# Kernel tuning notes

Measured on AMD Instinct MI355X. Metric: run time of the kernel, lower is better.

Reference implementation:

```python
import jax, jax.numpy as jnp
import numpy as np

BUCKETS = 16


def conv2d(x, w, b):
    # x: [N, Cin, H, W], w: [Cout, Cin, kh, kw], stride 1, padding 1
    y = jax.lax.conv_general_dilated(
        x, w, window_strides=(1, 1), padding=((1, 1), (1, 1)),
        dimension_numbers=("NCHW", "OIHW", "NCHW"))
    return y + b[None, :, None, None]


def setup_inputs() -> dict:
    key = jax.random.key(0)
    k1, k2, k3, k4, k5 = jax.random.split(key, 5)
    x = jax.random.normal(k1, (32, 64, 112, 112), dtype=jnp.float32)
    W = jax.random.normal(k2, (128, 64, 3, 3), dtype=jnp.float32) * 0.05
    b = jax.random.normal(k3, (128,), dtype=jnp.float32) * 0.05
    b2 = jax.random.normal(k4, (128,), dtype=jnp.float32) * 0.05  # hashed_conv's own bias
    hashed_weights = jax.random.normal(k5, (BUCKETS,), dtype=jnp.float32)
    return {"x": x, "W": W, "b": b, "b2": b2, "hashed_weights": hashed_weights}


def reference(x, W, b, b2, hashed_weights):
    out = conv2d(x, W, b)
    # thresholds derived from min/max of the ORIGINAL weights
    wmax = jnp.max(W)
    wmin = jnp.min(W)
    step = (wmax - wmin) / BUCKETS
    # sequential per-bucket replacement (faithful to in-place loop semantics:
    # values replaced at bucket i are re-compared against later thresholds)
    hw = W
    for i in range(BUCKETS):
        thr = (i + 1) * step + wmin
        hw = jnp.where(hw > thr, hashed_weights[i], hw)
    hashed_out = conv2d(x, hw, b2)
    return (out, hashed_out)
```

## Files before the change

### kernel.cpp

```cpp
#include <hip/hip_runtime.h>
#include <stdint.h>

#define CIN 64
#define HHW 112
#define NPIX 12544
#define COUT 128
#define KTOT 576
#define NBUCKETS 16

typedef __attribute__((ext_vector_type(8))) short s8v;
typedef __attribute__((ext_vector_type(4))) float f4v;
typedef __attribute__((ext_vector_type(8))) unsigned short u8v;

__device__ __forceinline__ unsigned short f2bf(float f) {
  unsigned int u = __float_as_uint(f);
  unsigned int r = (u + 0x7fffu + ((u >> 16) & 1u)) >> 16;
  return (unsigned short)r;
}

__device__ __forceinline__ void gload_lds16(const void* g, void* l) {
  __builtin_amdgcn_global_load_lds(
      (const __attribute__((address_space(1))) unsigned int*)g,
      (__attribute__((address_space(3))) unsigned int*)l, 16, 0, 0);
}

__global__ __launch_bounds__(1024) void hashedconv_prep_kernel(
    const float* __restrict__ W, const float* __restrict__ hashed_w,
    unsigned short* __restrict__ W2, unsigned short* __restrict__ zp) {
  const int NW = COUT * CIN * 9;
  int tid = threadIdx.x;
  if (zp && tid < 128) zp[tid] = 0;
  float vmin = 1e30f, vmax = -1e30f;
  for (int i = tid; i < NW; i += 1024) {
    float v = W[i];
    vmin = fminf(vmin, v);
    vmax = fmaxf(vmax, v);
  }
  #pragma unroll
  for (int off = 32; off > 0; off >>= 1) {
    vmin = fminf(vmin, __shfl_down(vmin, off, 64));
    vmax = fmaxf(vmax, __shfl_down(vmax, off, 64));
  }
  __shared__ float smin[16], smax[16];
  __shared__ float s_wmin, s_step;
  __shared__ float hv[NBUCKETS];
  int wave = tid >> 6, lane = tid & 63;
  if (lane == 0) { smin[wave] = vmin; smax[wave] = vmax; }
  if (tid < NBUCKETS) hv[tid] = hashed_w[tid];
  __syncthreads();
  if (tid == 0) {
    float m = smin[0], M = smax[0];
    #pragma unroll
    for (int i = 1; i < 16; ++i) { m = fminf(m, smin[i]); M = fmaxf(M, smax[i]); }
    s_wmin = m;
    s_step = (M - m) / (float)NBUCKETS;
  }
  __syncthreads();
  float wmin = s_wmin, step = s_step;
  for (int i = tid; i < NW; i += 1024) {
    float v = W[i];
    int co  = i / 576;
    int rem = i - co * 576;
    int cin = rem / 9;
    int off = rem - cin * 9;
    float h = v;
    #pragma unroll
    for (int b = 0; b < NBUCKETS; ++b) {
      float thr = (float)(b + 1) * step + wmin;
      if (h > thr) h = hv[b];
    }
    int oidx = co * KTOT + off * 64 + cin;
    W2[oidx]               = f2bf(v);
    W2[COUT * KTOT + oidx] = f2bf(h);
  }
}

__global__ __launch_bounds__(256) void xpose_kernel(
    const float* __restrict__ x, unsigned short* __restrict__ xb) {
  __shared__ unsigned short t[64][264];
  const int n = blockIdx.y, p0 = blockIdx.x * 256, tid = threadIdx.x;
  const float* xp = x + (size_t)n * CIN * NPIX + p0;
  #pragma unroll
  for (int c = 0; c < 64; ++c)
    t[c][tid] = f2bf(xp[(size_t)c * NPIX + tid]);
  __syncthreads();
  unsigned short* ob = xb + ((size_t)n * NPIX + p0) * 64;
  #pragma unroll
  for (int it = 0; it < 8; ++it) {
    int u = it * 256 + tid;
    int px = u >> 3, slot = u & 7;
    u8v v;
    #pragma unroll
    for (int k = 0; k < 8; ++k) v[k] = t[slot * 8 + k][px];
    *(u8v*)(ob + (size_t)u * 8) = v;
  }
}

#define XS_PIXPAD 352
#define XS_SHORTS (XS_PIXPAD * 64)
#define HALF_SHORTS (128 * 32)

__global__ __launch_bounds__(256, 2) void hashedconv_mfma_kernel(
    const unsigned short* __restrict__ xb, const unsigned short* __restrict__ W2,
    const float* __restrict__ b, const float* __restrict__ b2,
    const unsigned short* __restrict__ zp, float* __restrict__ out,
    size_t out_half) {
  __shared__ __attribute__((aligned(16))) short lds[XS_SHORTS + 4 * HALF_SHORTS];
  short* xs = lds;
  short* ring = lds + XS_SHORTS;

  const int tid = threadIdx.x;
  const int bx = blockIdx.x;
  const int n  = blockIdx.y;
  const int hf = blockIdx.z;
  const int ty = bx / 7, tx = bx - ty * 7;
  const int h0 = ty * 16, w0 = tx * 16;
  const int lane = tid & 63, wv = tid >> 6;
  const int wr = wv >> 1;
  const int wcn = wv & 1;
  const int lrow = lane & 15, g = lane >> 4;

  const unsigned short* Wh = W2 + (size_t)hf * COUT * KTOT;

  #pragma unroll
  for (int it = 0; it < 11; ++it) {
    int u = it * 256 + tid;
    int pix = u >> 3, slot = u & 7;
    int py = pix / 18, px = pix - py * 18;
    int gh = h0 - 1 + py, gw = w0 - 1 + px;
    bool inb = (pix < 324) & (gh >= 0) & (gh < HHW) & (gw >= 0) & (gw < HHW);
    int srcslot = slot ^ (pix & 7);
    const unsigned short* gsrc = inb
        ? xb + (((size_t)n * NPIX + gh * HHW + gw) * 64 + srcslot * 8)
        : zp + srcslot * 8;
    gload_lds16(gsrc, xs + (size_t)(it * 256 + wv * 64) * 8);
  }

  auto stage_half = [&](int h) {
    short* buf = ring + (size_t)(h & 3) * HALF_SHORTS;
    const unsigned short* src = Wh + (h >> 1) * 64 + (h & 1) * 32;
    #pragma unroll
    for (int j = 0; j < 2; ++j) {
      int u = j * 256 + tid;
      int row = u >> 2, slot = u & 3;
      int srcs = slot ^ (row & 3);
      gload_lds16(src + (size_t)row * KTOT + srcs * 8,
                  buf + (size_t)(j * 256 + wv * 64) * 8);
    }
  };
  stage_half(0);
  stage_half(1);
  stage_half(2);

  f4v acc[4][8];
  #pragma unroll
  for (int i = 0; i < 4; ++i)
    #pragma unroll
    for (int j = 0; j < 8; ++j) acc[i][j] = (f4v)(0.f);

  int pyv[8], pxv[8];
  #pragma unroll
  for (int nt = 0; nt < 8; ++nt) {
    int p = wcn * 128 + nt * 16 + lrow;
    pyv[nt] = p >> 4; pxv[nt] = p & 15;
  }

#define PHASE(h_, VM)                                                        \
  {                                                                          \
    asm volatile("s_waitcnt vmcnt(" #VM ")" ::: "memory");                   \
    __builtin_amdgcn_s_barrier();                                            \
    const int h = (h_);                                                      \
    const short* wbuf = ring + (size_t)(h & 3) * HALF_SHORTS;                \
    const int ch = h >> 1;                                                   \
    const int dh = ch / 3, dw = ch - dh * 3;                                 \
    const int kofs = (h & 1) * 32 + g * 8;                                   \
    s8v af[4], bfv[8];                                                       \
    _Pragma("unroll") for (int mt = 0; mt < 4; ++mt) {                       \
      int row = wr * 64 + mt * 16 + lrow;                                    \
      af[mt] = *(const s8v*)(wbuf + row * 32 + (g ^ (row & 3)) * 8);         \
    }                                                                        \
    _Pragma("unroll") for (int nt = 0; nt < 8; ++nt) {                       \
      int s = (pyv[nt] + dh) * 18 + pxv[nt] + dw;                            \
      bfv[nt] = *(const s8v*)(xs + s * 64 + (kofs ^ ((s & 7) << 3)));        \
    }                                                                        \
    if (h + 3 <= 17) stage_half(h + 3);                                      \
    asm volatile("s_waitcnt lgkmcnt(0)" ::: "memory");                       \
    __builtin_amdgcn_sched_barrier(0);                                       \
    __builtin_amdgcn_s_setprio(1);                                           \
    _Pragma("unroll") for (int mt = 0; mt < 4; ++mt)                         \
      _Pragma("unroll") for (int nt = 0; nt < 8; ++nt)                       \
        acc[mt][nt] = __builtin_amdgcn_mfma_f32_16x16x32_bf16(               \
            af[mt], bfv[nt], acc[mt][nt], 0, 0, 0);                          \
    __builtin_amdgcn_s_setprio(0);                                           \
    __builtin_amdgcn_sched_barrier(0);                                       \
  }

  for (int c = 0; c < 8; ++c) {
    PHASE(2 * c, 4);
    PHASE(2 * c + 1, 4);
  }
  PHASE(16, 2);
  PHASE(17, 0);
#undef PHASE

  const float* bias = hf ? b2 : b;
  float* obase = out + (size_t)hf * out_half + (size_t)n * COUT * NPIX;
  #pragma unroll
  for (int mt = 0; mt < 4; ++mt) {
    #pragma unroll
    for (int r = 0; r < 4; ++r) {
      int co = wr * 64 + mt * 16 + g * 4 + r;
      float bv = bias[co];
      #pragma unroll
      for (int nt = 0; nt < 8; ++nt) {
        int p = wcn * 128 + nt * 16 + lrow;
        int h = h0 + (p >> 4), w = w0 + (p & 15);
        obase[(size_t)co * NPIX + h * HHW + w] = acc[mt][nt][r] + bv;
      }
    }
  }
}

__global__ __launch_bounds__(256) void hashedconv_fb_kernel(
    const float* __restrict__ x, const unsigned short* __restrict__ W2,
    const float* __restrict__ b, const float* __restrict__ b2,
    float* __restrict__ out, size_t out_half) {
  __shared__ __attribute__((aligned(16))) short lds[11520 + 8192];
  short* xs = lds;
  short* wcs = lds + 11520;
  const int tid = threadIdx.x;
  const int bx = blockIdx.x;
  const int n  = blockIdx.y;
  const int hf = blockIdx.z;
  const int ty = bx / 7, tx = bx - ty * 7;
  const int h0 = ty * 8, w0 = tx * 16;
  const int lane = tid & 63, wv = tid >> 6;
  const int wr = wv >> 1, wcn = wv & 1;
  const int lrow = lane & 15, g = lane >> 4;
  f4v acc[4][4];
  #pragma unroll
  for (int i = 0; i < 4; ++i)
    #pragma unroll
    for (int j = 0; j < 4; ++j) acc[i][j] = (f4v)(0.f);
  const float* xn = x + (size_t)n * CIN * NPIX;
  for (int u = tid; u < 1440; u += 256) {
    int cg = u / 180;
    int pix = u - cg * 180;
    int pyp = pix / 18, pxp = pix - pyp * 18;
    int gh = h0 - 1 + pyp, gw = w0 - 1 + pxp;
    bool inb = (gh >= 0) & (gh < HHW) & (gw >= 0) & (gw < HHW);
    const float* xp = xn + (size_t)(cg * 8) * NPIX + gh * HHW + gw;
    s8v pk;
    #pragma unroll
    for (int cc = 0; cc < 8; ++cc) {
      float v = inb ? xp[(size_t)cc * NPIX] : 0.f;
      pk[cc] = (short)f2bf(v);
    }
    *(s8v*)(xs + pix * 64 + ((cg * 8) ^ ((pix & 7) << 3))) = pk;
  }
  const unsigned short* Wh = W2 + (size_t)hf * COUT * KTOT;
  for (int c = 0; c < 9; ++c) {
    #pragma unroll
    for (int j = 0; j < 4; ++j) {
      int u = tid + j * 256;
      int row = u >> 3, slot = u & 7;
      s8v v = *(const s8v*)(Wh + (size_t)row * KTOT + c * 64 + slot * 8);
      *(s8v*)(wcs + row * 64 + ((slot * 8) ^ ((row & 7) << 3))) = v;
    }
    __syncthreads();
    int dh = c / 3, dw = c - dh * 3;
    #pragma unroll
    for (int kh2 = 0; kh2 < 2; ++kh2) {
      int kofs = kh2 * 32 + g * 8;
      s8v af[4], bfv[4];
      #pragma unroll
      for (int mt = 0; mt < 4; ++mt) {
        int row = wr * 64 + mt * 16 + lrow;
        af[mt] = *(const s8v*)(wcs + row * 64 + (kofs ^ ((row & 7) << 3)));
      }
      #pragma unroll
      for (int nt = 0; nt < 4; ++nt) {
        int p = wcn * 64 + nt * 16 + lrow;
        int s = ((p >> 4) + dh) * 18 + ((p & 15) + dw);
        bfv[nt] = *(const s8v*)(xs + s * 64 + (kofs ^ ((s & 7) << 3)));
      }
      #pragma unroll
      for (int mt = 0; mt < 4; ++mt)
        #pragma unroll
        for (int nt = 0; nt < 4; ++nt)
          acc[mt][nt] = __builtin_amdgcn_mfma_f32_16x16x32_bf16(
              af[mt], bfv[nt], acc[mt][nt], 0, 0, 0);
    }
    __syncthreads();
  }
  const float* bias = hf ? b2 : b;
  float* obase = out + (size_t)hf * out_half + (size_t)n * COUT * NPIX;
  #pragma unroll
  for (int mt = 0; mt < 4; ++mt) {
    #pragma unroll
    for (int r = 0; r < 4; ++r) {
      int co = wr * 64 + mt * 16 + g * 4 + r;
      float bv = bias[co];
      #pragma unroll
      for (int nt = 0; nt < 4; ++nt) {
        int p = wcn * 64 + nt * 16 + lrow;
        int h = h0 + (p >> 4), w = w0 + (p & 15);
        obase[(size_t)co * NPIX + h * HHW + w] = acc[mt][nt][r] + bv;
      }
    }
  }
}

extern "C" void kernel_launch(void* const* d_in, const int* in_sizes, int n_in,
                              void* d_out, int out_size, void* d_ws, size_t ws_size,
                              hipStream_t stream) {
  const float* x      = (const float*)d_in[0];
  const float* W      = (const float*)d_in[1];
  const float* b      = (const float*)d_in[2];
  const float* b2     = (const float*)d_in[3];
  const float* hashed = (const float*)d_in[4];
  float* out = (float*)d_out;

  const int N = in_sizes[0] / (CIN * NPIX);
  const size_t out_half = (size_t)N * COUT * NPIX;
  const size_t XB_SHORTS = (size_t)N * NPIX * 64;
  const size_t need = (XB_SHORTS + 2 * COUT * KTOT) * 2 + 256;

  if (ws_size >= need) {
    unsigned short* xb = (unsigned short*)d_ws;
    unsigned short* W2 = xb + XB_SHORTS;
    unsigned short* zp = W2 + 2 * COUT * KTOT;
    hipLaunchKernelGGL(hashedconv_prep_kernel, dim3(1), dim3(1024), 0, stream,
                       W, hashed, W2, zp);
    hipLaunchKernelGGL(xpose_kernel, dim3(NPIX / 256, N), dim3(256), 0, stream,
                       x, xb);
    hipLaunchKernelGGL(hashedconv_mfma_kernel, dim3(49, N, 2), dim3(256), 0,
                       stream, xb, W2, b, b2, zp, out, out_half);
  } else {
    unsigned short* W2 = (unsigned short*)d_ws;
    hipLaunchKernelGGL(hashedconv_prep_kernel, dim3(1), dim3(1024), 0, stream,
                       W, hashed, W2, (unsigned short*)nullptr);
    hipLaunchKernelGGL(hashedconv_fb_kernel, dim3(98, N, 2), dim3(256), 0,
                       stream, x, W2, b, b2, out, out_half);
  }
}
```

Before: 269.4 us.

## Double-buffer MFMA operand fragments to prefetch next phase's LDS reads

Operand fragments are now double-buffered in registers. Each phase issues the LDS reads for the next K-chunk before running the MFMAs of the current one, which removes the lgkmcnt(0) stall between the reads and the matrix ops. The global-to-LDS wait loosens from vmcnt(4) to vmcnt(2) so the next chunk's ring slot is ready one phase earlier. Pixel row and column coordinates are folded into a single precomputed LDS base index. The cost is roughly 48 more live VGPRs, which could lower occupancy or cause spills.

```diff
diff --git a/kernel.cpp b/kernel.cpp
--- a/kernel.cpp
+++ b/kernel.cpp
@@ -158,50 +158,72 @@
     #pragma unroll
     for (int j = 0; j < 8; ++j) acc[i][j] = (f4v)(0.f);
 
-  int pyv[8], pxv[8];
+  int sbase[8];
   #pragma unroll
   for (int nt = 0; nt < 8; ++nt) {
     int p = wcn * 128 + nt * 16 + lrow;
-    pyv[nt] = p >> 4; pxv[nt] = p & 15;
-  }
-
-#define PHASE(h_, VM)                                                        \
+    sbase[nt] = (p >> 4) * 18 + (p & 15);
+  }
+
+  s8v af0[4], bf0[8], af1[4], bf1[8];
+
+#define READS(hh, AF, BF)                                                    \
+  if ((hh) <= 17) {                                                          \
+    const int h__ = (hh);                                                    \
+    const short* wbuf__ = ring + (size_t)(h__ & 3) * HALF_SHORTS;            \
+    const int ch__ = h__ >> 1;                                               \
+    const int dh__ = ch__ / 3, dw__ = ch__ - dh__ * 3;                       \
+    const int kofs__ = (h__ & 1) * 32 + g * 8;                               \
+    _Pragma("unroll") for (int mt = 0; mt < 4; ++mt) {                       \
+      int row = wr * 64 + mt * 16 + lrow;                                    \
+      AF[mt] = *(const s8v*)(wbuf__ + row * 32 + (g ^ (row & 3)) * 8);       \
+    }                                                                        \
+    _Pragma("unroll") for (int nt = 0; nt < 8; ++nt) {                       \
+      int s = sbase[nt] + dh__ * 18 + dw__;                                  \
+      BF[nt] = *(const s8v*)(xs + s * 64 + (kofs__ ^ ((s & 7) << 3)));       \
+    }                                                                        \
+  }
+
+#define PHASE(h_, VM, AFC, BFC, AFN, BFN)                                    \
   {                                                                          \
     asm volatile("s_waitcnt vmcnt(" #VM ")" ::: "memory");                   \
     __builtin_amdgcn_s_barrier();                                            \
-    const int h = (h_);                                                      \
-    const short* wbuf = ring + (size_t)(h & 3) * HALF_SHORTS;                \
-    const int ch = h >> 1;                                                   \
-    const int dh = ch / 3, dw = ch - dh * 3;                                 \
-    const int kofs = (h & 1) * 32 + g * 8;                                   \
-    s8v af[4], bfv[8];                                                       \
-    _Pragma("unroll") for (int mt = 0; mt < 4; ++mt) {                       \
-      int row = wr * 64 + mt * 16 + lrow;                                    \
-      af[mt] = *(const s8v*)(wbuf + row * 32 + (g ^ (row & 3)) * 8);         \
-    }                                                                        \
-    _Pragma("unroll") for (int nt = 0; nt < 8; ++nt) {                       \
-      int s = (pyv[nt] + dh) * 18 + pxv[nt] + dw;                            \
-      bfv[nt] = *(const s8v*)(xs + s * 64 + (kofs ^ ((s & 7) << 3)));        \
-    }                                                                        \
-    if (h + 3 <= 17) stage_half(h + 3);                                      \
-    asm volatile("s_waitcnt lgkmcnt(0)" ::: "memory");                       \
+    READS((h_) + 1, AFN, BFN);                                               \
+    if ((h_) + 3 <= 17) stage_half((h_) + 3);                                \
     __builtin_amdgcn_sched_barrier(0);                                       \
     __builtin_amdgcn_s_setprio(1);                                           \
     _Pragma("unroll") for (int mt = 0; mt < 4; ++mt)                         \
       _Pragma("unroll") for (int nt = 0; nt < 8; ++nt)                       \
         acc[mt][nt] = __builtin_amdgcn_mfma_f32_16x16x32_bf16(               \
-            af[mt], bfv[nt], acc[mt][nt], 0, 0, 0);                          \
+            AFC[mt], BFC[nt], acc[mt][nt], 0, 0, 0);                         \
     __builtin_amdgcn_s_setprio(0);                                           \
     __builtin_amdgcn_sched_barrier(0);                                       \
   }
 
-  for (int c = 0; c < 8; ++c) {
-    PHASE(2 * c, 4);
-    PHASE(2 * c + 1, 4);
-  }
-  PHASE(16, 2);
-  PHASE(17, 0);
+  asm volatile("s_waitcnt vmcnt(4)" ::: "memory");
+  __builtin_amdgcn_s_barrier();
+  READS(0, af0, bf0);
+
+  PHASE(0,  2, af0, bf0, af1, bf1);
+  PHASE(1,  2, af1, bf1, af0, bf0);
+  PHASE(2,  2, af0, bf0, af1, bf1);
+  PHASE(3,  2, af1, bf1, af0, bf0);
+  PHASE(4,  2, af0, bf0, af1, bf1);
+  PHASE(5,  2, af1, bf1, af0, bf0);
+  PHASE(6,  2, af0, bf0, af1, bf1);
+  PHASE(7,  2, af1, bf1, af0, bf0);
+  PHASE(8,  2, af0, bf0, af1, bf1);
+  PHASE(9,  2, af1, bf1, af0, bf0);
+  PHASE(10, 2, af0, bf0, af1, bf1);
+  PHASE(11, 2, af1, bf1, af0, bf0);
+  PHASE(12, 2, af0, bf0, af1, bf1);
+  PHASE(13, 2, af1, bf1, af0, bf0);
+  PHASE(14, 2, af0, bf0, af1, bf1);
+  PHASE(15, 2, af1, bf1, af0, bf0);
+  PHASE(16, 0, af0, bf0, af1, bf1);
+  PHASE(17, 0, af1, bf1, af0, bf0);
 #undef PHASE
+#undef READS
 
   const float* bias = hf ? b2 : b;
   float* obase = out + (size_t)hf * out_half + (size_t)n * COUT * NPIX;
```

Result: slower. 373.7 us (+38.7%).
